# Performance work log

Measured on AMD Instinct MI355X. Metric: run time of the kernel, lower is better.

Reference implementation:

```python
import jax, jax.numpy as jnp
import numpy as np

B, L, D, K_F = 2, 1024, 768, 16  # batch, seq_len, n_embd, num_eigh**2
N_FFT = 2048


def setup_inputs() -> dict:
    key = jax.random.key(0)
    k1, k2, k3, k4 = jax.random.split(key, 4)
    x = jax.random.normal(k1, (B, L, D), dtype=jnp.float32)
    phi = jax.random.normal(k2, (L, K_F), dtype=jnp.float32) * 0.1
    M_phi_plus = jax.random.normal(k3, (K_F, D, D), dtype=jnp.float32) * (1.0 / np.sqrt(K_F * D))
    M_phi_minus = jax.random.normal(k4, (K_F, D, D), dtype=jnp.float32) * (1.0 / np.sqrt(K_F * D))
    return {"x": x, "phi": phi, "M_phi_plus": M_phi_plus, "M_phi_minus": M_phi_minus, "n": N_FFT}


def _convolve(u, v, n):
    """FFT causal convolution with K spectral filters (flash-stu `convolve`, use_approx=False).
    u: [B, L, D] inputs; v: [L, K] filters; n: FFT length (>= 2L-1 padded pow2).
    Returns U_plus, U_minus: [B, L, K, D].
    """
    b, l, d = u.shape
    sgn = jnp.where(jnp.arange(l) % 2 == 0, 1.0, -1.0).astype(u.dtype)  # alternating +/-
    # Stack the plain and sign-modulated signals: [B, L, 1, D, 2]
    U = jnp.stack([u, u * sgn[None, :, None]], axis=-1)[:, :, None, :, :]
    Uf = jnp.fft.rfft(U, n=n, axis=1)                      # [B, F, 1, D, 2] complex
    vf = jnp.fft.rfft(v, n=n, axis=0)[None, :, :, None, None]  # [1, F, K, 1, 1]
    conv = jnp.fft.irfft(vf * Uf, n=n, axis=1)[:, :l]      # [B, L, K, D, 2]
    U_plus = conv[..., 0]
    U_minus = conv[..., 1] * sgn[None, :, None, None]
    return U_plus, U_minus


def reference(x, phi, M_phi_plus, M_phi_minus, n):
    U_plus, U_minus = _convolve(x, phi, n)
    # tensordot(U, M, dims=([2,3],[0,2])): contract eigenmode k and input channel i
    spectral_plus = jnp.einsum('blki,koi->blo', U_plus, M_phi_plus)
    spectral_minus = jnp.einsum('blki,koi->blo', U_minus, M_phi_minus)
    return spectral_plus + spectral_minus
```

## Files before the change

kernel.cpp:

```cpp
#include <hip/hip_runtime.h>
#include <hip/hip_fp16.h>

typedef unsigned short u16;
typedef unsigned int   u32;
typedef _Float16 f16;
typedef __attribute__((ext_vector_type(8))) f16 f16x8;
typedef __attribute__((ext_vector_type(2))) __fp16 fp16x2;
typedef __attribute__((ext_vector_type(4))) float f32x4;

#define B_SZ  2
#define L_SEQ 1024
#define D_EMB 768
#define KF    16
#define MDIM  (B_SZ * L_SEQ)
#define KROW  (KF * D_EMB)
#define MELEM ((size_t)KF * D_EMB * D_EMB)
#define NTILE 96
#define PT_SZ 16384

__device__ __forceinline__ void gload16(const void* g, void* l) {
    __builtin_amdgcn_global_load_lds(
        (const __attribute__((address_space(1))) u32*)g,
        (__attribute__((address_space(3))) u32*)l, 16, 0, 0);
}

#define VMCNT6() asm volatile("s_waitcnt vmcnt(6)" ::: "memory")
#define VMCNT0() asm volatile("s_waitcnt vmcnt(0)" ::: "memory")

__global__ __launch_bounds__(256) void stu_setup(const float* __restrict__ x,
                                                 const float* __restrict__ phi,
                                                 u16* __restrict__ xT,
                                                 u16* __restrict__ Ttab) {
    __shared__ __align__(16) float xs[64][68];
    const int bid = blockIdx.x;
    const int tid = threadIdx.x;

    if (bid < 384) {
        const int s0 = (bid & 15) << 6;
        const int d0 = ((bid >> 4) % 12) << 6;
        const int b  = bid / 192;

#pragma unroll
        for (int j = 0; j < 4; ++j) {
            int c = tid + (j << 8);
            int row = c >> 4;
            int col = (c & 15) << 2;
            *(float4*)&xs[row][col] =
                *(const float4*)&x[((size_t)b * L_SEQ + s0 + row) * D_EMB + d0 + col];
        }
        __syncthreads();

        const int dl = tid >> 2;
        const int ss = (tid & 3) << 4;
        const int dg = d0 + dl;
        const int xorv = (dg & 7) << 3;

        union { u16 v[16]; uint4 q[2]; } pk;
#pragma unroll
        for (int u = 0; u < 16; ++u)
            pk.v[u] = __half_as_ushort(__float2half(xs[ss + u][dl]));

        size_t base = (size_t)b * D_EMB * L_SEQ + (size_t)dg * L_SEQ + s0;
        *(uint4*)&xT[base + ( ss      ^ xorv)] = pk.q[0];
        *(uint4*)&xT[base + ((ss + 8) ^ xorv)] = pk.q[1];
    } else {
        const int f = bid - 384;
        const int q = f & 15;
        const int k = f >> 4;
        const int tt  = tid >> 2;
        const int ss0 = (tid & 3) << 4;

        union { u16 v[16]; uint4 q4[2]; } pk;
#pragma unroll
        for (int u = 0; u < 16; ++u) {
            int s = (q << 6) + tt - (ss0 + u);
            float v = (s >= 0 && s < L_SEQ) ? phi[s * KF + k] : 0.f;
            pk.v[u] = __half_as_ushort(__float2half(v));
        }
        const int xorv = (tt & 7) << 3;
        u16* tile = Ttab + (((size_t)k * 16 + q) << 12);
        *(uint4*)&tile[(tt << 6) + ( ss0      ^ xorv)] = pk.q4[0];
        *(uint4*)&tile[(tt << 6) + ((ss0 + 8) ^ xorv)] = pk.q4[1];
    }
}

__global__ __launch_bounds__(256) void stu_conv_mcvt(
        const u16* __restrict__ xT, const u16* __restrict__ Ttab,
        u16* __restrict__ Up, u16* __restrict__ Um,
        const float* __restrict__ Mp, const float* __restrict__ Mm,
        u16* __restrict__ Hp, u16* __restrict__ Hm) {
    __shared__ __align__(16) u16 Xs[2][128 * 64];
    __shared__ __align__(16) u16 Tps[2][64 * 64];

    const int bid = blockIdx.x;
    const int tid = threadIdx.x;

    if (bid < 512) {
        const size_t n8 = MELEM / 8;
        size_t i = (size_t)bid * 256 + tid;
        const size_t stride = (size_t)512 * 256;
        for (size_t cc = i; cc < n8; cc += stride) {
            const size_t g = cc << 3;
            {
                const float4 a0 = *(const float4*)&Mp[g];
                const float4 a1 = *(const float4*)&Mp[g + 4];
                union { fp16x2 h2[4]; uint4 q; } u;
                u.h2[0] = __builtin_amdgcn_cvt_pkrtz(a0.x, a0.y);
                u.h2[1] = __builtin_amdgcn_cvt_pkrtz(a0.z, a0.w);
                u.h2[2] = __builtin_amdgcn_cvt_pkrtz(a1.x, a1.y);
                u.h2[3] = __builtin_amdgcn_cvt_pkrtz(a1.z, a1.w);
                *(uint4*)&Hp[g] = u.q;
            }
            {
                const float4 a0 = *(const float4*)&Mm[g];
                const float4 a1 = *(const float4*)&Mm[g + 4];
                union { fp16x2 h2[4]; uint4 q; } u;
                u.h2[0] = __builtin_amdgcn_cvt_pkrtz(a0.x, a0.y);
                u.h2[1] = __builtin_amdgcn_cvt_pkrtz(a0.z, a0.w);
                u.h2[2] = __builtin_amdgcn_cvt_pkrtz(a1.x, a1.y);
                u.h2[3] = __builtin_amdgcn_cvt_pkrtz(a1.z, a1.w);
                *(uint4*)&Hm[g] = u.q;
            }
        }
        return;
    }

    const int c    = bid - 512;
    const int xcd  = c & 7;
    const int w    = c >> 3;
    const int ti   = 15 - (w / 24);
    const int t0   = ti << 6;
    const int inner = w % 24;
    const int bk   = (xcd << 2) + (inner / 6);
    const int b    = bk >> 4;
    const int k    = bk & 15;
    const int d0   = (inner % 6) << 7;

    const int lane = tid & 63;
    const int wid  = tid >> 6;
    const int wr   = wid >> 1;
    const int wc   = wid & 1;
    const int lr   = lane & 15;
    const int lk   = lane >> 4;

    const u32 xm = (lr & 1) ? 0x00008000u : 0x80000000u;

    f32x4 acc[2][2][4];
#pragma unroll
    for (int s = 0; s < 2; ++s)
#pragma unroll
        for (int m = 0; m < 2; ++m)
#pragma unroll
            for (int n = 0; n < 4; ++n)
                acc[s][m][n] = (f32x4){0.f, 0.f, 0.f, 0.f};

    const u16* xTb = xT + (size_t)b * D_EMB * L_SEQ + (size_t)d0 * L_SEQ;
    const u16* Tpk = Ttab + ((size_t)k << 16);

    auto stageX = [&](int buf, int r0) {
#pragma unroll
        for (int j = 0; j < 4; ++j) {
            int cc = tid + (j << 8);
            gload16(xTb + (size_t)(cc >> 3) * L_SEQ + r0 + ((cc & 7) << 3),
                    &Xs[buf][cc << 3]);
        }
    };
    auto stageT = [&](int buf, int q) {
        const u16* tp = Tpk + ((size_t)q << 12);
        gload16(tp + (tid << 3),         &Tps[buf][tid << 3]);
        gload16(tp + ((tid + 256) << 3), &Tps[buf][(tid + 256) << 3]);
    };

    stageX(0, 0);
    stageT(0, ti);

    int cur = 0;
    for (int r0 = 0; r0 <= t0; r0 += 64) {
        const int more = (r0 < t0);
        if (more) {
            stageT(cur ^ 1, ((t0 - r0) >> 6) - 1);
            stageX(cur ^ 1, r0 + 64);
        }
        if (more) { VMCNT6(); } else { VMCNT0(); }
        __builtin_amdgcn_s_barrier();

        const char* XsC = (const char*)&Xs[cur][0];
        const char* TpC = (const char*)&Tps[cur][0];

#pragma unroll
        for (int kk = 0; kk < 2; ++kk) {
            f16x8 bfr[4];
#pragma unroll
            for (int n = 0; n < 4; ++n) {
                const int row = (wc << 6) + (n << 4) + lr;
                const int boff = ((kk << 6) + (lk << 4)) ^ ((row & 7) << 4);
                bfr[n] = *(const f16x8*)(XsC + row * 128 + boff);
            }
#pragma unroll
            for (int m = 0; m < 2; ++m) {
                const int rowt = (wr << 5) + (m << 4) + lr;
                const int aoff = ((kk << 6) + (lk << 4)) ^ ((rowt & 7) << 4);
                const f16x8 ap = *(const f16x8*)(TpC + rowt * 128 + aoff);
                union { f16x8 h; u32 wv[4]; } cv;
                cv.h = ap;
#pragma unroll
                for (int qd = 0; qd < 4; ++qd) cv.wv[qd] ^= xm;
                const f16x8 am = cv.h;
#pragma unroll
                for (int n = 0; n < 4; ++n) {
                    acc[0][m][n] = __builtin_amdgcn_mfma_f32_16x16x32_f16(
                        ap, bfr[n], acc[0][m][n], 0, 0, 0);
                    acc[1][m][n] = __builtin_amdgcn_mfma_f32_16x16x32_f16(
                        am, bfr[n], acc[1][m][n], 0, 0, 0);
                }
            }
        }
        __builtin_amdgcn_s_barrier();
        cur ^= 1;
    }

#pragma unroll
    for (int m = 0; m < 2; ++m) {
        const int trow = t0 + (wr << 5) + (m << 4) + (lk << 2);
#pragma unroll
        for (int n = 0; n < 4; ++n) {
            const int col = d0 + (wc << 6) + (n << 4) + lr;
#pragma unroll
            for (int j = 0; j < 4; ++j) {
                size_t idx = ((size_t)(b * L_SEQ + trow + j) * KF + k) * D_EMB + col;
                Up[idx] = __half_as_ushort(__float2half(acc[0][m][n][j]));
                Um[idx] = __half_as_ushort(__float2half(acc[1][m][n][j]));
            }
        }
    }
}

__global__ __launch_bounds__(256) void stu_spectral_mfma(
        const u16* __restrict__ Up, const u16* __restrict__ Um,
        const u16* __restrict__ Mhp, const u16* __restrict__ Mhm,
        float* __restrict__ out, u16* __restrict__ P, int usePartial) {
    __shared__ __align__(16) u16 As[128 * 64];
    __shared__ __align__(16) u16 Bs[128 * 64];

    const int h   = blockIdx.x;
    const int z   = h & 7;
    const int rem = h >> 3;
    const int o0  = (rem % 6) << 7;
    const int m0  = (rem / 6) << 7;
    const int sign = z & 1;
    const int k0 = (z >> 1) << 2;

    const u16* A    = sign ? Um : Up;
    const u16* Bsrc = sign ? Mhm : Mhp;

    const int tid  = threadIdx.x;
    const int lane = tid & 63;
    const int wid  = tid >> 6;
    const int wr   = wid >> 1;
    const int wc   = wid & 1;
    const int lr   = lane & 15;
    const int lk   = lane >> 4;

    f32x4 acc[4][4];
#pragma unroll
    for (int m = 0; m < 4; ++m)
#pragma unroll
        for (int n = 0; n < 4; ++n)
            acc[m][n] = (f32x4){0.f, 0.f, 0.f, 0.f};

    for (int k = k0; k < k0 + 4; ++k) {
        const u16* Ak = A + (size_t)m0 * KROW + k * D_EMB;
        const u16* Bk = Bsrc + (size_t)k * D_EMB * D_EMB + (size_t)o0 * D_EMB;

        for (int ic = 0; ic < D_EMB; ic += 64) {
            __syncthreads();
#pragma unroll
            for (int j = 0; j < 4; ++j) {
                const int c = tid + (j << 8);
                const int row = c >> 3;
                const int off = ((c & 7) ^ (row & 7)) << 3;
                gload16(Ak + (size_t)row * KROW + ic + off, &As[c << 3]);
                gload16(Bk + (size_t)row * D_EMB + ic + off, &Bs[c << 3]);
            }
            __syncthreads();

#pragma unroll
            for (int kk = 0; kk < 2; ++kk) {
                f16x8 af[4], bf[4];
#pragma unroll
                for (int m = 0; m < 4; ++m) {
                    const int row = wr * 64 + (m << 4) + lr;
                    const int boff = (((kk << 2) + lk) ^ (row & 7)) << 4;
                    af[m] = *(const f16x8*)((const char*)&As[0] + row * 128 + boff);
                }
#pragma unroll
                for (int n = 0; n < 4; ++n) {
                    const int row = wc * 64 + (n << 4) + lr;
                    const int boff = (((kk << 2) + lk) ^ (row & 7)) << 4;
                    bf[n] = *(const f16x8*)((const char*)&Bs[0] + row * 128 + boff);
                }
#pragma unroll
                for (int m = 0; m < 4; ++m)
#pragma unroll
                    for (int n = 0; n < 4; ++n)
                        acc[m][n] = __builtin_amdgcn_mfma_f32_16x16x32_f16(
                            af[m], bf[n], acc[m][n], 0, 0, 0);
            }
        }
    }

    if (usePartial) {
        u16* Pt = P + (size_t)h * PT_SZ;
#pragma unroll
        for (int m = 0; m < 4; ++m) {
            const int rowl = wr * 64 + (m << 4) + (lk << 2);
#pragma unroll
            for (int n = 0; n < 4; ++n) {
                const int coll = wc * 64 + (n << 4) + lr;
#pragma unroll
                for (int j = 0; j < 4; ++j)
                    Pt[(rowl + j) * 128 + coll] =
                        __half_as_ushort(__float2half(acc[m][n][j]));
            }
        }
    } else {
#pragma unroll
        for (int m = 0; m < 4; ++m) {
            const int row = m0 + wr * 64 + (m << 4) + (lk << 2);
#pragma unroll
            for (int n = 0; n < 4; ++n) {
                const int col = o0 + wc * 64 + (n << 4) + lr;
#pragma unroll
                for (int j = 0; j < 4; ++j)
                    atomicAdd(&out[(size_t)(row + j) * D_EMB + col], acc[m][n][j]);
            }
        }
    }
}

__global__ __launch_bounds__(256) void stu_reduce(const u16* __restrict__ P,
                                                  float* __restrict__ out) {
    const int g    = blockIdx.x * 256 + threadIdx.x;
    const int row  = g / 96;
    const int col0 = (g % 96) << 3;
    const int tile = (row >> 7) * 6 + (col0 >> 7);
    const u16* p = P + (size_t)tile * 8 * PT_SZ + ((row & 127) << 7) + (col0 & 127);

    float s[8] = {0.f, 0.f, 0.f, 0.f, 0.f, 0.f, 0.f, 0.f};
#pragma unroll
    for (int z = 0; z < 8; ++z) {
        const uint4 q = *(const uint4*)(p + (size_t)z * PT_SZ);
        union { uint4 q; u16 v[8]; } u;
        u.q = q;
#pragma unroll
        for (int j = 0; j < 8; ++j)
            s[j] += __half2float(__ushort_as_half(u.v[j]));
    }
    const size_t ob = (size_t)row * D_EMB + col0;
    *(float4*)&out[ob]     = (float4){s[0], s[1], s[2], s[3]};
    *(float4*)&out[ob + 4] = (float4){s[4], s[5], s[6], s[7]};
}

extern "C" void kernel_launch(void* const* d_in, const int* in_sizes, int n_in,
                              void* d_out, int out_size, void* d_ws, size_t ws_size,
                              hipStream_t stream) {
    const float* x   = (const float*)d_in[0];
    const float* phi = (const float*)d_in[1];
    const float* Mp  = (const float*)d_in[2];
    const float* Mm  = (const float*)d_in[3];
    float* out = (float*)d_out;

    const size_t S = (size_t)MDIM * KROW;
    u16* Up   = (u16*)d_ws;
    u16* Um   = Up + S;
    u16* Mhp  = Um + S;
    u16* Mhm  = Mhp + MELEM;
    u16* xT   = Mhm + MELEM;
    u16* Ttab = xT + (size_t)B_SZ * D_EMB * L_SEQ;
    u16* Part = Ttab + (size_t)KF * 16 * 4096;

    const size_t elems_needed = 2 * S + 2 * MELEM + 1572864 + 1048576 + 12582912;
    const int usePartial = (ws_size >= elems_needed * sizeof(u16)) ? 1 : 0;

    if (!usePartial)
        (void)hipMemsetAsync(d_out, 0, (size_t)out_size * sizeof(float), stream);

    stu_setup<<<dim3(640), dim3(256), 0, stream>>>(x, phi, xT, Ttab);

    stu_conv_mcvt<<<dim3(3584), dim3(256), 0, stream>>>(
        xT, Ttab, Up, Um, Mp, Mm, Mhp, Mhm);

    stu_spectral_mfma<<<dim3(NTILE * 8), dim3(256), 0, stream>>>(
        Up, Um, Mhp, Mhm, out, Part, usePartial);

    if (usePartial)
        stu_reduce<<<dim3(768), dim3(256), 0, stream>>>(Part, out);
}
```

Before: 164.7 us.

## Enlarge spectral GEMM tile to 256 rows and double split-K factor

The spectral MFMA kernel now computes a 256x128 output tile per block (two 128-row sub-tiles sharing each B fragment) instead of 128x128, and splits the K reduction 16 ways instead of 8, keeping the block count at 768. This reuses each loaded M tile across twice as many rows, cutting B-side global and LDS traffic per FLOP. The cost is twice the accumulator registers (possible occupancy loss or spills), double the LDS for A, and a partial buffer and reduce pass twice as large with 16 fp16 partials summed per output.

New measurement: 211.0 us. +28.1%, slower.

```diff
diff --git a/kernel.cpp b/kernel.cpp
--- a/kernel.cpp
+++ b/kernel.cpp
@@ -15,8 +15,7 @@
 #define MDIM  (B_SZ * L_SEQ)
 #define KROW  (KF * D_EMB)
 #define MELEM ((size_t)KF * D_EMB * D_EMB)
-#define NTILE 96
-#define PT_SZ 16384
+#define PT3   32768
 
 __device__ __forceinline__ void gload16(const void* g, void* l) {
     __builtin_amdgcn_global_load_lds(
@@ -239,16 +238,16 @@
         const u16* __restrict__ Up, const u16* __restrict__ Um,
         const u16* __restrict__ Mhp, const u16* __restrict__ Mhm,
         float* __restrict__ out, u16* __restrict__ P, int usePartial) {
-    __shared__ __align__(16) u16 As[128 * 64];
+    __shared__ __align__(16) u16 As[256 * 64];
     __shared__ __align__(16) u16 Bs[128 * 64];
 
     const int h   = blockIdx.x;
-    const int z   = h & 7;
-    const int rem = h >> 3;
+    const int z   = h & 15;
+    const int rem = h >> 4;
     const int o0  = (rem % 6) << 7;
-    const int m0  = (rem / 6) << 7;
+    const int m0  = (rem / 6) << 8;
     const int sign = z & 1;
-    const int k0 = (z >> 1) << 2;
+    const int k0 = (z >> 1) << 1;
 
     const u16* A    = sign ? Um : Up;
     const u16* Bsrc = sign ? Mhm : Mhp;
@@ -261,38 +260,40 @@
     const int lr   = lane & 15;
     const int lk   = lane >> 4;
 
-    f32x4 acc[4][4];
-#pragma unroll
-    for (int m = 0; m < 4; ++m)
-#pragma unroll
-        for (int n = 0; n < 4; ++n)
-            acc[m][n] = (f32x4){0.f, 0.f, 0.f, 0.f};
-
-    for (int k = k0; k < k0 + 4; ++k) {
+    f32x4 acc[2][4][4];
+#pragma unroll
+    for (int s = 0; s < 2; ++s)
+#pragma unroll
+        for (int m = 0; m < 4; ++m)
+#pragma unroll
+            for (int n = 0; n < 4; ++n)
+                acc[s][m][n] = (f32x4){0.f, 0.f, 0.f, 0.f};
+
+    for (int k = k0; k < k0 + 2; ++k) {
         const u16* Ak = A + (size_t)m0 * KROW + k * D_EMB;
         const u16* Bk = Bsrc + (size_t)k * D_EMB * D_EMB + (size_t)o0 * D_EMB;
 
         for (int ic = 0; ic < D_EMB; ic += 64) {
             __syncthreads();
+#pragma unroll
+            for (int j = 0; j < 8; ++j) {
+                const int c = tid + (j << 8);
+                const int row = c >> 3;
+                const int off = ((c & 7) ^ (row & 7)) << 3;
+                gload16(Ak + (size_t)row * KROW + ic + off, &As[c << 3]);
+            }
 #pragma unroll
             for (int j = 0; j < 4; ++j) {
                 const int c = tid + (j << 8);
                 const int row = c >> 3;
                 const int off = ((c & 7) ^ (row & 7)) << 3;
-                gload16(Ak + (size_t)row * KROW + ic + off, &As[c << 3]);
                 gload16(Bk + (size_t)row * D_EMB + ic + off, &Bs[c << 3]);
             }
             __syncthreads();
 
 #pragma unroll
             for (int kk = 0; kk < 2; ++kk) {
-                f16x8 af[4], bf[4];
-#pragma unroll
-                for (int m = 0; m < 4; ++m) {
-                    const int row = wr * 64 + (m << 4) + lr;
-                    const int boff = (((kk << 2) + lk) ^ (row & 7)) << 4;
-                    af[m] = *(const f16x8*)((const char*)&As[0] + row * 128 + boff);
-                }
+                f16x8 bf[4];
 #pragma unroll
                 for (int n = 0; n < 4; ++n) {
                     const int row = wc * 64 + (n << 4) + lr;
@@ -300,41 +301,56 @@
                     bf[n] = *(const f16x8*)((const char*)&Bs[0] + row * 128 + boff);
                 }
 #pragma unroll
-                for (int m = 0; m < 4; ++m)
-#pragma unroll
-                    for (int n = 0; n < 4; ++n)
-                        acc[m][n] = __builtin_amdgcn_mfma_f32_16x16x32_f16(
-                            af[m], bf[n], acc[m][n], 0, 0, 0);
+                for (int s = 0; s < 2; ++s) {
+                    f16x8 af[4];
+#pragma unroll
+                    for (int m = 0; m < 4; ++m) {
+                        const int row = (s << 7) + wr * 64 + (m << 4) + lr;
+                        const int boff = (((kk << 2) + lk) ^ (row & 7)) << 4;
+                        af[m] = *(const f16x8*)((const char*)&As[0] + row * 128 + boff);
+                    }
+#pragma unroll
+                    for (int m = 0; m < 4; ++m)
+#pragma unroll
+                        for (int n = 0; n < 4; ++n)
+                            acc[s][m][n] = __builtin_amdgcn_mfma_f32_16x16x32_f16(
+                                af[m], bf[n], acc[s][m][n], 0, 0, 0);
+                }
             }
         }
     }
 
     if (usePartial) {
-        u16* Pt = P + (size_t)h * PT_SZ;
-#pragma unroll
-        for (int m = 0; m < 4; ++m) {
-            const int rowl = wr * 64 + (m << 4) + (lk << 2);
-#pragma unroll
-            for (int n = 0; n < 4; ++n) {
-                const int coll = wc * 64 + (n << 4) + lr;
-#pragma unroll
-                for (int j = 0; j < 4; ++j)
-                    Pt[(rowl + j) * 128 + coll] =
-                        __half_as_ushort(__float2half(acc[m][n][j]));
-            }
-        }
+        u16* Pt = P + (size_t)h * PT3;
+#pragma unroll
+        for (int s = 0; s < 2; ++s)
+#pragma unroll
+            for (int m = 0; m < 4; ++m) {
+                const int rowl = (s << 7) + wr * 64 + (m << 4) + (lk << 2);
+#pragma unroll
+                for (int n = 0; n < 4; ++n) {
+                    const int coll = wc * 64 + (n << 4) + lr;
+#pragma unroll
+                    for (int j = 0; j < 4; ++j)
+                        Pt[(rowl + j) * 128 + coll] =
+                            __half_as_ushort(__float2half(acc[s][m][n][j]));
+                }
+            }
     } else {
 #pragma unroll
-        for (int m = 0; m < 4; ++m) {
-            const int row = m0 + wr * 64 + (m << 4) + (lk << 2);
-#pragma unroll
-            for (int n = 0; n < 4; ++n) {
-                const int col = o0 + wc * 64 + (n << 4) + lr;
-#pragma unroll
-                for (int j = 0; j < 4; ++j)
-                    atomicAdd(&out[(size_t)(row + j) * D_EMB + col], acc[m][n][j]);
-            }
-        }
+        for (int s = 0; s < 2; ++s)
+#pragma unroll
+            for (int m = 0; m < 4; ++m) {
+                const int row = m0 + (s << 7) + wr * 64 + (m << 4) + (lk << 2);
+#pragma unroll
+                for (int n = 0; n < 4; ++n) {
+                    const int col = o0 + wc * 64 + (n << 4) + lr;
+#pragma unroll
+                    for (int j = 0; j < 4; ++j)
+                        atomicAdd(&out[(size_t)(row + j) * D_EMB + col],
+                                  acc[s][m][n][j]);
+                }
+            }
     }
 }
 
@@ -343,13 +359,13 @@
     const int g    = blockIdx.x * 256 + threadIdx.x;
     const int row  = g / 96;
     const int col0 = (g % 96) << 3;
-    const int tile = (row >> 7) * 6 + (col0 >> 7);
-    const u16* p = P + (size_t)tile * 8 * PT_SZ + ((row & 127) << 7) + (col0 & 127);
+    const int tile = (row >> 8) * 6 + (col0 >> 7);
+    const u16* p = P + ((size_t)tile << 4) * PT3 + ((row & 255) << 7) + (col0 & 127);
 
     float s[8] = {0.f, 0.f, 0.f, 0.f, 0.f, 0.f, 0.f, 0.f};
 #pragma unroll
-    for (int z = 0; z < 8; ++z) {
-        const uint4 q = *(const uint4*)(p + (size_t)z * PT_SZ);
+    for (int z = 0; z < 16; ++z) {
+        const uint4 q = *(const uint4*)(p + (size_t)z * PT3);
         union { uint4 q; u16 v[8]; } u;
         u.q = q;
 #pragma unroll
@@ -379,7 +395,7 @@
     u16* Ttab = xT + (size_t)B_SZ * D_EMB * L_SEQ;
     u16* Part = Ttab + (size_t)KF * 16 * 4096;
 
-    const size_t elems_needed = 2 * S + 2 * MELEM + 1572864 + 1048576 + 12582912;
+    const size_t elems_needed = 2 * S + 2 * MELEM + 1572864 + 1048576 + 25165824;
     const int usePartial = (ws_size >= elems_needed * sizeof(u16)) ? 1 : 0;
 
     if (!usePartial)
@@ -390,7 +406,7 @@
     stu_conv_mcvt<<<dim3(3584), dim3(256), 0, stream>>>(
         xT, Ttab, Up, Um, Mp, Mm, Mhp, Mhm);
 
-    stu_spectral_mfma<<<dim3(NTILE * 8), dim3(256), 0, stream>>>(
+    stu_spectral_mfma<<<dim3(768), dim3(256), 0, stream>>>(
         Up, Um, Mhp, Mhm, out, Part, usePartial);
 
     if (usePartial)
```
